# Performance work log

Measured on AMD Instinct MI355X. Metric: run time of the kernel, lower is better.

## Reference

```python
import jax, jax.numpy as jnp
import numpy as np
from jax import lax

B, T = 2, 2048
HID = 2048
H, K, KC = 16, 128, 4
D = H * K  # projection dim
EPS = 1e-5
SCALE = K ** -0.5


def causal_conv_silu(x, w, b):
    # x: [B,T,D], depthwise causal conv, w: [D,KC], b: [D]
    xp = jnp.pad(jnp.swapaxes(x, 1, 2), ((0, 0), (0, 0), (KC - 1, 0)))  # [B,D,T+KC-1]
    y = lax.conv_general_dilated(xp, w[:, None, :], (1,), 'VALID', feature_group_count=D)
    return jax.nn.silu(jnp.swapaxes(y, 1, 2) + b)


def l2norm(x):
    return x * lax.rsqrt(jnp.sum(x * x, -1, keepdims=True) + 1e-6)


def kda_scan(q, k, v, g, beta):
    # gated delta-rule linear recurrence (KDA), per-key-dim log decay g
    # q,k,v,g: [B,T,H,K]; beta: [B,T,H]
    qT, kT, vT, gT, bT = (jnp.moveaxis(a, 1, 0) for a in (q, k, v, g, beta))
    S0 = jnp.zeros((q.shape[0], H, K, K), q.dtype)  # state [B,H,K,V]

    def step(S, inp):
        qt, kt, vt, gt, bt = inp
        S = S * jnp.exp(gt)[..., None]                                   # decay along K
        vd = (vt - jnp.einsum('bhkv,bhk->bhv', S, kt)) * bt[..., None]   # delta-rule error * beta
        S = S + kt[..., None] * vd[:, :, None, :]                        # rank-1 update
        return S, jnp.einsum('bhkv,bhk->bhv', S, qt)

    _, o = lax.scan(step, S0, (qT, kT, vT, gT, bT))
    return jnp.moveaxis(o, 0, 1)  # [B,T,H,K]


def _forward(x, Wq, Wk, Wv, conv_q_w, conv_q_b, conv_k_w, conv_k_b, conv_v_w, conv_v_b,
             Wfa, Wfb, A_log, dt_bias, Wb, Wga, Wgb, o_norm_w, Wo):
    b, t = x.shape[:2]
    q = causal_conv_silu(x @ Wq, conv_q_w, conv_q_b).reshape(b, t, H, K)
    k = causal_conv_silu(x @ Wk, conv_k_w, conv_k_b).reshape(b, t, H, K)
    v = causal_conv_silu(x @ Wv, conv_v_w, conv_v_b).reshape(b, t, H, K)
    # fine-grained decay gate: g = -exp(A_log[h]) * softplus(f_b(f_a(x)) + dt_bias)
    g = jax.nn.softplus((x @ Wfa) @ Wfb + dt_bias).reshape(b, t, H, K)
    g = -jnp.exp(A_log)[None, None, :, None] * g
    beta = jax.nn.sigmoid(x @ Wb)  # [B,T,H]
    q = l2norm(q) * SCALE
    k = l2norm(k)
    o = kda_scan(q, k, v, g, beta)  # [B,T,H,K]
    # gated head-wise RMSNorm
    gate = ((x @ Wga) @ Wgb).reshape(b, t, H, K)
    var = jnp.mean(o * o, -1, keepdims=True)
    o = o * lax.rsqrt(var + EPS) * o_norm_w * jax.nn.sigmoid(gate)
    return o.reshape(b, t, D) @ Wo


def setup_inputs() -> dict:
    key = jax.random.key(0)
    ks = jax.random.split(key, 16)
    s = 0.02
    f32 = jnp.float32
    return {
        'x': jax.random.normal(ks[0], (B, T, HID), f32),
        'Wq': jax.random.normal(ks[1], (HID, D), f32) * s,
        'Wk': jax.random.normal(ks[2], (HID, D), f32) * s,
        'Wv': jax.random.normal(ks[3], (HID, D), f32) * s,
        'conv_q_w': jax.random.normal(ks[4], (D, KC), f32) * 0.2,
        'conv_q_b': jnp.zeros((D,), f32),
        'conv_k_w': jax.random.normal(ks[5], (D, KC), f32) * 0.2,
        'conv_k_b': jnp.zeros((D,), f32),
        'conv_v_w': jax.random.normal(ks[6], (D, KC), f32) * 0.2,
        'conv_v_b': jnp.zeros((D,), f32),
        'Wfa': jax.random.normal(ks[7], (HID, K), f32) * s,
        'Wfb': jax.random.normal(ks[8], (K, D), f32) * s,
        'A_log': jnp.log(jax.random.uniform(ks[9], (H,), f32, 1.0, 16.0)),
        'dt_bias': jnp.zeros((D,), f32),
        'Wb': jax.random.normal(ks[10], (HID, H), f32) * s,
        'Wga': jax.random.normal(ks[11], (HID, K), f32) * s,
        'Wgb': jax.random.normal(ks[12], (K, D), f32) * s,
        'o_norm_w': jnp.ones((K,), f32),
        'Wo': jax.random.normal(ks[13], (D, HID), f32) * s,
    }


def reference(x, Wq, Wk, Wv, conv_q_w, conv_q_b, conv_k_w, conv_k_b, conv_v_w, conv_v_b,
              Wfa, Wfb, A_log, dt_bias, Wb, Wga, Wgb, o_norm_w, Wo):
    return _forward(x, Wq, Wk, Wv, conv_q_w, conv_q_b, conv_k_w, conv_k_b, conv_v_w, conv_v_b,
                    Wfa, Wfb, A_log, dt_bias, Wb, Wga, Wgb, o_norm_w, Wo)
```

## Files before the change

### kernel.cpp

```cpp
#include <hip/hip_runtime.h>
#include <cstddef>

#define Bsz 2
#define Tt  2048
#define HIDc 2048
#define Hh  16
#define Kc  128
#define Dc  2048
#define BT  (Bsz*Tt)
#define TS  8
#define FGBs 384

typedef __attribute__((ext_vector_type(8))) __bf16 bf16x8;
typedef __attribute__((ext_vector_type(4))) __bf16 bf16x4;
typedef __attribute__((ext_vector_type(4))) float f32x4;

__device__ __forceinline__ float epilogue(float vacc, int c, int mode,
                                          const float* __restrict__ alog,
                                          const float* __restrict__ dtb) {
    if (mode == 1) {
        float z  = vacc + dtb[c];
        float sp = fmaxf(z, 0.f) + log1pf(expf(-fabsf(z)));
        return expf(-expf(alog[c >> 7]) * sp);
    } else if (mode == 3) {
        return (c >= 256) ? 1.f / (1.f + expf(-vacc)) : vacc;
    }
    return vacc;
}

__global__ __launch_bounds__(256) void gemm_bf16_mfma(
    const __bf16* __restrict__ A, const __bf16* __restrict__ Bw,
    float* __restrict__ C, __bf16* __restrict__ C2,
    int M, int N, int K, int lda, int mode,
    const float* __restrict__ alog, const float* __restrict__ dtb)
{
    __shared__ __bf16 As[128 * 64];
    __shared__ __bf16 Bs[128 * 64];
    const int tid = threadIdx.x;
    const int lane = tid & 63;
    const int wave = tid >> 6;
    const int wr = wave >> 1, wc = wave & 1;
    const int l15 = lane & 15, g = lane >> 4;
    const int row0 = blockIdx.y * 128, col0 = blockIdx.x * 128;

    f32x4 acc[4][4];
#pragma unroll
    for (int m = 0; m < 4; m++)
#pragma unroll
        for (int n = 0; n < 4; n++)
            acc[m][n] = (f32x4){0.f, 0.f, 0.f, 0.f};

    for (int k0 = 0; k0 < K; k0 += 64) {
        __syncthreads();
#pragma unroll
        for (int i = 0; i < 4; i++) {
            const int c = i * 256 + tid;
            const int row = c >> 3, kc = c & 7;
            const int scol = k0 + 8 * (kc ^ (row & 7));
            __builtin_amdgcn_global_load_lds(
                (const __attribute__((address_space(1))) void*)(A + (size_t)(row0 + row) * lda + scol),
                (__attribute__((address_space(3))) void*)(As + (size_t)(i * 256 + (tid & ~63)) * 8),
                16, 0, 0);
        }
#pragma unroll
        for (int i = 0; i < 4; i++) {
            const int c = i * 256 + tid;
            const int row = c >> 3, kc = c & 7;
            const int scol = k0 + 8 * (kc ^ (row & 7));
            __builtin_amdgcn_global_load_lds(
                (const __attribute__((address_space(1))) void*)(Bw + (size_t)(col0 + row) * K + scol),
                (__attribute__((address_space(3))) void*)(Bs + (size_t)(i * 256 + (tid & ~63)) * 8),
                16, 0, 0);
        }
        __syncthreads();
#pragma unroll
        for (int ks = 0; ks < 2; ks++) {
            bf16x8 af[4], bfr[4];
#pragma unroll
            for (int m = 0; m < 4; m++) {
                const int row = wr * 64 + m * 16 + l15;
                const int kc = ks * 4 + g;
                af[m] = *(const bf16x8*)(As + row * 64 + 8 * (kc ^ (row & 7)));
            }
#pragma unroll
            for (int n = 0; n < 4; n++) {
                const int col = wc * 64 + n * 16 + l15;
                const int kc = ks * 4 + g;
                bfr[n] = *(const bf16x8*)(Bs + col * 64 + 8 * (kc ^ (col & 7)));
            }
#pragma unroll
            for (int m = 0; m < 4; m++)
#pragma unroll
                for (int n = 0; n < 4; n++)
                    acc[m][n] = __builtin_amdgcn_mfma_f32_16x16x32_bf16(
                        af[m], bfr[n], acc[m][n], 0, 0, 0);
        }
    }
#pragma unroll
    for (int m = 0; m < 4; m++) {
        const int rbase = row0 + wr * 64 + m * 16 + g * 4;
#pragma unroll
        for (int n = 0; n < 4; n++) {
            const int col = col0 + wc * 64 + n * 16 + l15;
#pragma unroll
            for (int r = 0; r < 4; r++) {
                const float val = epilogue(acc[m][n][r], col, mode, alog, dtb);
                C[(size_t)(rbase + r) * N + col] = val;
                if (C2) C2[(size_t)(rbase + r) * N + col] = (__bf16)val;
            }
        }
    }
}

__global__ __launch_bounds__(256) void cvt_bf16(
    const float* __restrict__ in, __bf16* __restrict__ o)
{
    const int i = blockIdx.x * 256 + threadIdx.x;
    float4 v = *(const float4*)(in + (size_t)4 * i);
    bf16x4 r;
    r[0] = (__bf16)v.x; r[1] = (__bf16)v.y; r[2] = (__bf16)v.z; r[3] = (__bf16)v.w;
    *(bf16x4*)(o + (size_t)4 * i) = r;
}

__global__ __launch_bounds__(256) void transpose_to_bf16(
    const float* __restrict__ W, __bf16* __restrict__ WT, int Kd, int N)
{
    __shared__ float tile[32][33];
    const int n0 = blockIdx.x * 32, k0 = blockIdx.y * 32;
    const int tx = threadIdx.x & 31, ty = threadIdx.x >> 5;
#pragma unroll
    for (int i = 0; i < 4; i++)
        tile[ty + 8 * i][tx] = W[(size_t)(k0 + ty + 8 * i) * N + n0 + tx];
    __syncthreads();
#pragma unroll
    for (int i = 0; i < 4; i++)
        WT[(size_t)(n0 + ty + 8 * i) * Kd + k0 + tx] = (__bf16)tile[tx][ty + 8 * i];
}

__global__ __launch_bounds__(256) void pack_fgbT(
    const float* __restrict__ Wfa, const float* __restrict__ Wga,
    const float* __restrict__ Wb, __bf16* __restrict__ BcatT)
{
    const int i = blockIdx.x * 256 + threadIdx.x;
    if (i >= FGBs * HIDc) return;
    const int c = i / HIDc, k = i % HIDc;
    float v = 0.f;
    if (c < 128)      v = Wfa[(size_t)k * 128 + c];
    else if (c < 256) v = Wga[(size_t)k * 128 + (c - 128)];
    else if (c < 272) v = Wb[(size_t)k * 16 + (c - 256)];
    BcatT[i] = (__bf16)v;
}

__global__ __launch_bounds__(128) void conv_silu_norm(
    const float* __restrict__ pre, const float* __restrict__ cw,
    const float* __restrict__ cb, float* __restrict__ out, int mode)
{
    const int bid = blockIdx.x;
    const int h = bid & (Hh - 1);
    const int bt = bid >> 4;
    const int t = bt & (Tt - 1);
    const int lane = threadIdx.x;
    const int col = h * Kc + lane;
    const float w0 = cw[col * 4 + 0], w1 = cw[col * 4 + 1];
    const float w2 = cw[col * 4 + 2], w3 = cw[col * 4 + 3];
    const float* bp = pre + (size_t)bt * Dc + col;
    float acc = cb[col] + w3 * bp[0];
    if (t >= 1) acc += w2 * bp[-Dc];
    if (t >= 2) acc += w1 * bp[-2 * Dc];
    if (t >= 3) acc += w0 * bp[-3 * Dc];
    float val = acc / (1.f + expf(-acc));
    if (mode) {
        float ss = val * val;
#pragma unroll
        for (int m = 1; m < 64; m <<= 1) ss += __shfl_xor(ss, m);
        __shared__ float p2[2];
        if ((lane & 63) == 0) p2[lane >> 6] = ss;
        __syncthreads();
        float tot = p2[0] + p2[1];
        float r = rsqrtf(tot + 1e-6f);
        val *= r;
        if (mode == 2) val *= 0.08838834764831845f;
    }
    out[(size_t)bt * Dc + col] = val;
}

template <int CTRL>
__device__ __forceinline__ float dpp_add(float v) {
    return __int_as_float(__builtin_amdgcn_update_dpp(
        0, __float_as_int(v), CTRL, 0xf, 0xf, true));
}

__device__ __forceinline__ void reduce3_row(float& a, float& b, float& c) {
    a += dpp_add<0xB1>(a);
    b += dpp_add<0xB1>(b);
    c += dpp_add<0xB1>(c);
    a += dpp_add<0x4E>(a);
    b += dpp_add<0x4E>(b);
    c += dpp_add<0x4E>(c);
    a += dpp_add<0x124>(a);
    b += dpp_add<0x124>(b);
    c += dpp_add<0x124>(c);
    a += dpp_add<0x128>(a);
    b += dpp_add<0x128>(b);
    c += dpp_add<0x128>(c);
}

__device__ __forceinline__ float kda_step(
    const float4 cq[2], const float4 ck[2], const float4 cd[2],
    float cv, float cbt, float S[8])
{
    float kv0 = 0.f, kv1 = 0.f, qs0 = 0.f, qs1 = 0.f, qk0 = 0.f, qk1 = 0.f;
#pragma unroll
    for (int i = 0; i < 2; i++) {
        S[4 * i + 0] *= cd[i].x;
        S[4 * i + 1] *= cd[i].y;
        S[4 * i + 2] *= cd[i].z;
        S[4 * i + 3] *= cd[i].w;
        kv0 = fmaf(ck[i].x, S[4 * i + 0], kv0);
        kv1 = fmaf(ck[i].y, S[4 * i + 1], kv1);
        kv0 = fmaf(ck[i].z, S[4 * i + 2], kv0);
        kv1 = fmaf(ck[i].w, S[4 * i + 3], kv1);
        qs0 = fmaf(cq[i].x, S[4 * i + 0], qs0);
        qs1 = fmaf(cq[i].y, S[4 * i + 1], qs1);
        qs0 = fmaf(cq[i].z, S[4 * i + 2], qs0);
        qs1 = fmaf(cq[i].w, S[4 * i + 3], qs1);
        qk0 = fmaf(ck[i].x, cq[i].x, qk0);
        qk1 = fmaf(ck[i].y, cq[i].y, qk1);
        qk0 = fmaf(ck[i].z, cq[i].z, qk0);
        qk1 = fmaf(ck[i].w, cq[i].w, qk1);
    }
    float kv = kv0 + kv1, qs = qs0 + qs1, qk = qk0 + qk1;
    reduce3_row(kv, qs, qk);
    float vd = (cv - kv) * cbt;
    float ov = fmaf(qk, vd, qs);
#pragma unroll
    for (int i = 0; i < 2; i++) {
        S[4 * i + 0] = fmaf(ck[i].x, vd, S[4 * i + 0]);
        S[4 * i + 1] = fmaf(ck[i].y, vd, S[4 * i + 1]);
        S[4 * i + 2] = fmaf(ck[i].z, vd, S[4 * i + 2]);
        S[4 * i + 3] = fmaf(ck[i].w, vd, S[4 * i + 3]);
    }
    return ov;
}

__device__ __forceinline__ void kda_tile(
    const float (*sm)[TS * 128], const float* vm,
    const float* bm, float S[8], int kq, int vloc,
    float* __restrict__ op, int lane)
{
    float4 cq[2], ck[2], cd[2];
    float cv, cb;
#pragma unroll
    for (int i = 0; i < 2; i++) {
        cq[i] = *(const float4*)&sm[0][(kq * 2 + i) * 4];
        ck[i] = *(const float4*)&sm[1][(kq * 2 + i) * 4];
        cd[i] = *(const float4*)&sm[2][(kq * 2 + i) * 4];
    }
    cv = vm[vloc];
    cb = bm[0];
#pragma unroll
    for (int t = 0; t < TS; ++t) {
        float4 nq[2], nk[2], nd[2];
        float nv = 0.f, nb = 0.f;
        if (t + 1 < TS) {
#pragma unroll
            for (int i = 0; i < 2; i++) {
                nq[i] = *(const float4*)&sm[0][(t + 1) * 128 + (kq * 2 + i) * 4];
                nk[i] = *(const float4*)&sm[1][(t + 1) * 128 + (kq * 2 + i) * 4];
                nd[i] = *(const float4*)&sm[2][(t + 1) * 128 + (kq * 2 + i) * 4];
            }
            nv = vm[(t + 1) * 4 + vloc];
            nb = bm[t + 1];
        }
        const float ov = kda_step(cq, ck, cd, cv, cb, S);
        if ((lane & 15) == 0)
            op[(size_t)t * Dc + vloc] = ov;
        if (t + 1 < TS) {
#pragma unroll
            for (int i = 0; i < 2; i++) { cq[i] = nq[i]; ck[i] = nk[i]; cd[i] = nd[i]; }
            cv = nv; cb = nb;
        }
    }
}

__global__ __launch_bounds__(64, 2) void kda_scan_kernel(
    const float* __restrict__ q, const float* __restrict__ k,
    const float* __restrict__ v, const float* __restrict__ dec,
    const float* __restrict__ fgb, float* __restrict__ o)
{
    __shared__ float sA[3][TS * 128];
    __shared__ float sB[3][TS * 128];
    __shared__ float sC[3][TS * 128];
    __shared__ float vA[TS * 4], vB[TS * 4], vC[TS * 4];
    __shared__ float bA[TS], bB[TS], bC[TS];

    const int bid = blockIdx.x;
    const int r8 = bid & 7;
    const int s = bid >> 3;
    const int bh = r8 + 8 * (s >> 5);
    const int vc = s & 31;
    const int h = bh & (Hh - 1);
    const int b = bh >> 4;
    const int lane = threadIdx.x;
    const int vloc = lane >> 4;
    const int kq = lane & 15;
    const size_t base = ((size_t)b * Tt) * Dc + h * Kc;
    const size_t bbase = ((size_t)b * Tt) * FGBs + 256 + h;

    float S[8];
#pragma unroll
    for (int i = 0; i < 8; i++) S[i] = 0.f;

    const int s_t = lane >> 5;
    const int s_w = lane & 31;

#define STAGE(TILE, SM, VM, BM)                                                 \
    {                                                                           \
        _Pragma("unroll")                                                       \
        for (int r = 0; r < 4; r++) {                                           \
            const size_t rb = base + (size_t)((TILE) * TS + 2 * r + s_t) * Dc   \
                              + s_w * 4;                                        \
            __builtin_amdgcn_global_load_lds(                                   \
                (const __attribute__((address_space(1))) void*)(q + rb),        \
                (__attribute__((address_space(3))) void*)(&SM[0][r * 256]),     \
                16, 0, 0);                                                      \
            __builtin_amdgcn_global_load_lds(                                   \
                (const __attribute__((address_space(1))) void*)(k + rb),        \
                (__attribute__((address_space(3))) void*)(&SM[1][r * 256]),     \
                16, 0, 0);                                                      \
            __builtin_amdgcn_global_load_lds(                                   \
                (const __attribute__((address_space(1))) void*)(dec + rb),      \
                (__attribute__((address_space(3))) void*)(&SM[2][r * 256]),     \
                16, 0, 0);                                                      \
        }                                                                       \
        if (lane < 32)                                                          \
            __builtin_amdgcn_global_load_lds(                                   \
                (const __attribute__((address_space(1))) void*)(v + base        \
                    + (size_t)((TILE) * TS + (lane >> 2)) * Dc + vc * 4         \
                    + (lane & 3)),                                              \
                (__attribute__((address_space(3))) void*)(&VM[0]), 4, 0, 0);    \
        if (lane < TS)                                                          \
            __builtin_amdgcn_global_load_lds(                                   \
                (const __attribute__((address_space(1))) void*)(fgb + bbase     \
                    + (size_t)((TILE) * TS + lane) * FGBs),                     \
                (__attribute__((address_space(3))) void*)(&BM[0]), 4, 0, 0);    \
    }

    STAGE(0, sA, vA, bA);
    STAGE(1, sB, vB, bB);
    asm volatile("s_waitcnt vmcnt(14)" ::: "memory");
    __builtin_amdgcn_sched_barrier(0);

    const int NT = Tt / TS;
    for (int tile = 0; tile < NT; ++tile) {
        if (tile + 2 < NT) {
            const int r2 = (tile + 2) % 3;
            float (*sT)[TS * 128] = (r2 == 0) ? sA : (r2 == 1) ? sB : sC;
            float* vT = (r2 == 0) ? vA : (r2 == 1) ? vB : vC;
            float* bT = (r2 == 0) ? bA : (r2 == 1) ? bB : bC;
            STAGE(tile + 2, sT, vT, bT);
            __builtin_amdgcn_sched_barrier(0);
        }
        const int rr = tile % 3;
        const float (*sm)[TS * 128] = (rr == 0) ? sA : (rr == 1) ? sB : sC;
        const float* vm = (rr == 0) ? vA : (rr == 1) ? vB : vC;
        const float* bm = (rr == 0) ? bA : (rr == 1) ? bB : bC;
        kda_tile(sm, vm, bm, S, kq, vloc,
                 o + base + (size_t)tile * TS * Dc + vc * 4, lane);
        if (tile + 2 < NT)
            asm volatile("s_waitcnt vmcnt(22)" ::: "memory");
        else
            asm volatile("s_waitcnt vmcnt(8)" ::: "memory");
        __builtin_amdgcn_sched_barrier(0);
    }
#undef STAGE
}

__global__ __launch_bounds__(128) void post_norm(
    const float* __restrict__ o, const float* __restrict__ gate,
    const float* __restrict__ onw, __bf16* __restrict__ og)
{
    const int bid = blockIdx.x;
    const int h = bid & (Hh - 1);
    const int bt = bid >> 4;
    const int lane = threadIdx.x;
    size_t idx = (size_t)bt * Dc + h * Kc + lane;
    float ov = o[idx];
    float ss = ov * ov;
#pragma unroll
    for (int m = 1; m < 64; m <<= 1) ss += __shfl_xor(ss, m);
    __shared__ float p2[2];
    if ((lane & 63) == 0) p2[lane >> 6] = ss;
    __syncthreads();
    float var = (p2[0] + p2[1]) * (1.f / 128.f);
    float r = rsqrtf(var + 1e-5f);
    float gt = gate[idx];
    og[idx] = (__bf16)(ov * r * onw[lane] * (1.f / (1.f + expf(-gt))));
}

extern "C" void kernel_launch(void* const* d_in, const int* in_sizes, int n_in,
                              void* d_out, int out_size, void* d_ws, size_t ws_size,
                              hipStream_t stream) {
    const float* x        = (const float*)d_in[0];
    const float* Wq       = (const float*)d_in[1];
    const float* Wk       = (const float*)d_in[2];
    const float* Wv       = (const float*)d_in[3];
    const float* conv_q_w = (const float*)d_in[4];
    const float* conv_q_b = (const float*)d_in[5];
    const float* conv_k_w = (const float*)d_in[6];
    const float* conv_k_b = (const float*)d_in[7];
    const float* conv_v_w = (const float*)d_in[8];
    const float* conv_v_b = (const float*)d_in[9];
    const float* Wfa      = (const float*)d_in[10];
    const float* Wfb      = (const float*)d_in[11];
    const float* A_log    = (const float*)d_in[12];
    const float* dt_bias  = (const float*)d_in[13];
    const float* Wb       = (const float*)d_in[14];
    const float* Wga      = (const float*)d_in[15];
    const float* Wgb      = (const float*)d_in[16];
    const float* o_norm_w = (const float*)d_in[17];
    const float* Wo       = (const float*)d_in[18];
    float* out = (float*)d_out;

    float* ws = (float*)d_ws;
    const size_t SZ = (size_t)BT * Dc;
    float* bufA = ws + 0 * SZ;
    float* bufB = ws + 1 * SZ;
    float* bufC = ws + 2 * SZ;
    float* bufG = ws + 3 * SZ;
    float* bufQ = ws + 4 * SZ;
    float* bufI = ws + 5 * SZ;
    float* fgb  = ws + 6 * SZ;
    __bf16* fgb16 = (__bf16*)(fgb + (size_t)BT * FGBs);
    __bf16* xb    = fgb16 + (size_t)BT * FGBs;
    __bf16* wT    = xb + SZ;
    __bf16* BcatT = wT + (size_t)HIDc * Dc;

    dim3 blk(256);
    cvt_bf16<<<dim3(SZ / 1024), blk, 0, stream>>>(x, xb);
    pack_fgbT<<<dim3((FGBs * HIDc + 255) / 256), blk, 0, stream>>>(Wfa, Wga, Wb, BcatT);
    dim3 tgrid(Dc / 32, HIDc / 32);
    dim3 gbig(Dc / 128, BT / 128);
    transpose_to_bf16<<<tgrid, blk, 0, stream>>>(Wq, wT, HIDc, Dc);
    gemm_bf16_mfma<<<gbig, blk, 0, stream>>>(xb, wT, bufA, nullptr, BT, Dc, HIDc, HIDc, 0, nullptr, nullptr);
    transpose_to_bf16<<<tgrid, blk, 0, stream>>>(Wk, wT, HIDc, Dc);
    gemm_bf16_mfma<<<gbig, blk, 0, stream>>>(xb, wT, bufB, nullptr, BT, Dc, HIDc, HIDc, 0, nullptr, nullptr);
    transpose_to_bf16<<<tgrid, blk, 0, stream>>>(Wv, wT, HIDc, Dc);
    gemm_bf16_mfma<<<gbig, blk, 0, stream>>>(xb, wT, bufC, nullptr, BT, Dc, HIDc, HIDc, 0, nullptr, nullptr);
    dim3 gskin(FGBs / 128, BT / 128);
    gemm_bf16_mfma<<<gskin, blk, 0, stream>>>(xb, BcatT, fgb, fgb16, BT, FGBs, HIDc, HIDc, 3, nullptr, nullptr);
    dim3 tskin(Dc / 32, Kc / 32);
    transpose_to_bf16<<<tskin, blk, 0, stream>>>(Wfb, wT, Kc, Dc);
    gemm_bf16_mfma<<<gbig, blk, 0, stream>>>(fgb16, wT, bufG, nullptr, BT, Dc, Kc, FGBs, 1, A_log, dt_bias);
    transpose_to_bf16<<<tskin, blk, 0, stream>>>(Wgb, wT, Kc, Dc);
    gemm_bf16_mfma<<<gbig, blk, 0, stream>>>(fgb16 + 128, wT, bufI, nullptr, BT, Dc, Kc, FGBs, 0, nullptr, nullptr);
    dim3 cblk(128);
    dim3 cgrid(BT * Hh);
    conv_silu_norm<<<cgrid, cblk, 0, stream>>>(bufA, conv_q_w, conv_q_b, bufQ, 2);
    conv_silu_norm<<<cgrid, cblk, 0, stream>>>(bufB, conv_k_w, conv_k_b, bufA, 1);
    conv_silu_norm<<<cgrid, cblk, 0, stream>>>(bufC, conv_v_w, conv_v_b, bufB, 0);
    kda_scan_kernel<<<dim3(1024), dim3(64), 0, stream>>>(bufQ, bufA, bufB, bufG, fgb, bufC);
    post_norm<<<cgrid, cblk, 0, stream>>>(bufC, bufI, o_norm_w, xb);
    transpose_to_bf16<<<tgrid, blk, 0, stream>>>(Wo, wT, Dc, HIDc);
    dim3 gout(HIDc / 128, BT / 128);
    gemm_bf16_mfma<<<gout, blk, 0, stream>>>(xb, wT, out, nullptr, BT, HIDc, Dc, Dc, 0, nullptr, nullptr);
}
```

Baseline: 944.0 us.

## Batch QKV transposes and GEMMs into single launches; swizzle scan LDS reads

Merges the three Wq/Wk/Wv weight transposes and the three projection GEMMs into one launch each, using blockIdx.z to select the weight and output buffer. This gives a single 3x-larger grid that fills the GPU better and removes launch gaps. Separately, the scan kernel rotates each lane's LDS float4 slot by vloc to reduce bank conflicts among the four v-groups reading the same row. The cost is three transposed weight copies held in the workspace at once instead of one reused buffer.

Result: no change. 928.5 us (-1.6%).

```diff
diff --git a/kernel.cpp b/kernel.cpp
--- a/kernel.cpp
+++ b/kernel.cpp
@@ -29,13 +29,15 @@
 }
 
 __global__ __launch_bounds__(256) void gemm_bf16_mfma(
-    const __bf16* __restrict__ A, const __bf16* __restrict__ Bw,
-    float* __restrict__ C, __bf16* __restrict__ C2,
+    const __bf16* __restrict__ A, const __bf16* __restrict__ BwB, size_t bz,
+    float* __restrict__ CB, size_t cz, __bf16* __restrict__ C2,
     int M, int N, int K, int lda, int mode,
     const float* __restrict__ alog, const float* __restrict__ dtb)
 {
     __shared__ __bf16 As[128 * 64];
     __shared__ __bf16 Bs[128 * 64];
+    const __bf16* Bw = BwB + (size_t)blockIdx.z * bz;
+    float* C = CB + (size_t)blockIdx.z * cz;
     const int tid = threadIdx.x;
     const int lane = tid & 63;
     const int wave = tid >> 6;
@@ -126,6 +128,25 @@
     const float* __restrict__ W, __bf16* __restrict__ WT, int Kd, int N)
 {
     __shared__ float tile[32][33];
+    const int n0 = blockIdx.x * 32, k0 = blockIdx.y * 32;
+    const int tx = threadIdx.x & 31, ty = threadIdx.x >> 5;
+#pragma unroll
+    for (int i = 0; i < 4; i++)
+        tile[ty + 8 * i][tx] = W[(size_t)(k0 + ty + 8 * i) * N + n0 + tx];
+    __syncthreads();
+#pragma unroll
+    for (int i = 0; i < 4; i++)
+        WT[(size_t)(n0 + ty + 8 * i) * Kd + k0 + tx] = (__bf16)tile[tx][ty + 8 * i];
+}
+
+__global__ __launch_bounds__(256) void transpose3_to_bf16(
+    const float* __restrict__ W0, const float* __restrict__ W1,
+    const float* __restrict__ W2, __bf16* __restrict__ WTB, size_t wz,
+    int Kd, int N)
+{
+    __shared__ float tile[32][33];
+    const float* W = (blockIdx.z == 0) ? W0 : (blockIdx.z == 1) ? W1 : W2;
+    __bf16* WT = WTB + (size_t)blockIdx.z * wz;
     const int n0 = blockIdx.x * 32, k0 = blockIdx.y * 32;
     const int tx = threadIdx.x & 31, ty = threadIdx.x >> 5;
 #pragma unroll
@@ -245,17 +266,17 @@
 
 __device__ __forceinline__ void kda_tile(
     const float (*sm)[TS * 128], const float* vm,
-    const float* bm, float S[8], int kq, int vloc,
+    const float* bm, float S[8], int sl0, int sl1, int vloc,
     float* __restrict__ op, int lane)
 {
     float4 cq[2], ck[2], cd[2];
     float cv, cb;
-#pragma unroll
-    for (int i = 0; i < 2; i++) {
-        cq[i] = *(const float4*)&sm[0][(kq * 2 + i) * 4];
-        ck[i] = *(const float4*)&sm[1][(kq * 2 + i) * 4];
-        cd[i] = *(const float4*)&sm[2][(kq * 2 + i) * 4];
-    }
+    cq[0] = *(const float4*)&sm[0][sl0];
+    ck[0] = *(const float4*)&sm[1][sl0];
+    cd[0] = *(const float4*)&sm[2][sl0];
+    cq[1] = *(const float4*)&sm[0][sl1];
+    ck[1] = *(const float4*)&sm[1][sl1];
+    cd[1] = *(const float4*)&sm[2][sl1];
     cv = vm[vloc];
     cb = bm[0];
 #pragma unroll
@@ -263,12 +284,12 @@
         float4 nq[2], nk[2], nd[2];
         float nv = 0.f, nb = 0.f;
         if (t + 1 < TS) {
-#pragma unroll
-            for (int i = 0; i < 2; i++) {
-                nq[i] = *(const float4*)&sm[0][(t + 1) * 128 + (kq * 2 + i) * 4];
-                nk[i] = *(const float4*)&sm[1][(t + 1) * 128 + (kq * 2 + i) * 4];
-                nd[i] = *(const float4*)&sm[2][(t + 1) * 128 + (kq * 2 + i) * 4];
-            }
+            nq[0] = *(const float4*)&sm[0][(t + 1) * 128 + sl0];
+            nk[0] = *(const float4*)&sm[1][(t + 1) * 128 + sl0];
+            nd[0] = *(const float4*)&sm[2][(t + 1) * 128 + sl0];
+            nq[1] = *(const float4*)&sm[0][(t + 1) * 128 + sl1];
+            nk[1] = *(const float4*)&sm[1][(t + 1) * 128 + sl1];
+            nd[1] = *(const float4*)&sm[2][(t + 1) * 128 + sl1];
             nv = vm[(t + 1) * 4 + vloc];
             nb = bm[t + 1];
         }
@@ -304,6 +325,8 @@
     const int lane = threadIdx.x;
     const int vloc = lane >> 4;
     const int kq = lane & 15;
+    const int sl0 = ((kq * 2 + 0 + vloc) & 31) * 4;
+    const int sl1 = ((kq * 2 + 1 + vloc) & 31) * 4;
     const size_t base = ((size_t)b * Tt) * Dc + h * Kc;
     const size_t bbase = ((size_t)b * Tt) * FGBs + 256 + h;
 
@@ -365,7 +388,7 @@
         const float (*sm)[TS * 128] = (rr == 0) ? sA : (rr == 1) ? sB : sC;
         const float* vm = (rr == 0) ? vA : (rr == 1) ? vB : vC;
         const float* bm = (rr == 0) ? bA : (rr == 1) ? bB : bC;
-        kda_tile(sm, vm, bm, S, kq, vloc,
+        kda_tile(sm, vm, bm, S, sl0, sl1, vloc,
                  o + base + (size_t)tile * TS * Dc + vc * 4, lane);
         if (tile + 2 < NT)
             asm volatile("s_waitcnt vmcnt(22)" ::: "memory");
@@ -433,27 +456,29 @@
     float* fgb  = ws + 6 * SZ;
     __bf16* fgb16 = (__bf16*)(fgb + (size_t)BT * FGBs);
     __bf16* xb    = fgb16 + (size_t)BT * FGBs;
-    __bf16* wT    = xb + SZ;
-    __bf16* BcatT = wT + (size_t)HIDc * Dc;
+    __bf16* wT3   = xb + SZ;
+    __bf16* BcatT = wT3 + (size_t)3 * HIDc * Dc;
+    const size_t WZ = (size_t)HIDc * Dc;
 
     dim3 blk(256);
     cvt_bf16<<<dim3(SZ / 1024), blk, 0, stream>>>(x, xb);
     pack_fgbT<<<dim3((FGBs * HIDc + 255) / 256), blk, 0, stream>>>(Wfa, Wga, Wb, BcatT);
-    dim3 tgrid(Dc / 32, HIDc / 32);
-    dim3 gbig(Dc / 128, BT / 128);
-    transpose_to_bf16<<<tgrid, blk, 0, stream>>>(Wq, wT, HIDc, Dc);
-    gemm_bf16_mfma<<<gbig, blk, 0, stream>>>(xb, wT, bufA, nullptr, BT, Dc, HIDc, HIDc, 0, nullptr, nullptr);
-    transpose_to_bf16<<<tgrid, blk, 0, stream>>>(Wk, wT, HIDc, Dc);
-    gemm_bf16_mfma<<<gbig, blk, 0, stream>>>(xb, wT, bufB, nullptr, BT, Dc, HIDc, HIDc, 0, nullptr, nullptr);
-    transpose_to_bf16<<<tgrid, blk, 0, stream>>>(Wv, wT, HIDc, Dc);
-    gemm_bf16_mfma<<<gbig, blk, 0, stream>>>(xb, wT, bufC, nullptr, BT, Dc, HIDc, HIDc, 0, nullptr, nullptr);
-    dim3 gskin(FGBs / 128, BT / 128);
-    gemm_bf16_mfma<<<gskin, blk, 0, stream>>>(xb, BcatT, fgb, fgb16, BT, FGBs, HIDc, HIDc, 3, nullptr, nullptr);
+    dim3 tgrid3(Dc / 32, HIDc / 32, 3);
+    transpose3_to_bf16<<<tgrid3, blk, 0, stream>>>(Wq, Wk, Wv, wT3, WZ, HIDc, Dc);
+    dim3 gbig3(Dc / 128, BT / 128, 3);
+    gemm_bf16_mfma<<<gbig3, blk, 0, stream>>>(xb, wT3, WZ, bufA, SZ, nullptr,
+                                              BT, Dc, HIDc, HIDc, 0, nullptr, nullptr);
+    dim3 gskin(FGBs / 128, BT / 128, 1);
+    gemm_bf16_mfma<<<gskin, blk, 0, stream>>>(xb, BcatT, 0, fgb, 0, fgb16,
+                                              BT, FGBs, HIDc, HIDc, 3, nullptr, nullptr);
     dim3 tskin(Dc / 32, Kc / 32);
-    transpose_to_bf16<<<tskin, blk, 0, stream>>>(Wfb, wT, Kc, Dc);
-    gemm_bf16_mfma<<<gbig, blk, 0, stream>>>(fgb16, wT, bufG, nullptr, BT, Dc, Kc, FGBs, 1, A_log, dt_bias);
-    transpose_to_bf16<<<tskin, blk, 0, stream>>>(Wgb, wT, Kc, Dc);
-    gemm_bf16_mfma<<<gbig, blk, 0, stream>>>(fgb16 + 128, wT, bufI, nullptr, BT, Dc, Kc, FGBs, 0, nullptr, nullptr);
+    dim3 gbig(Dc / 128, BT / 128, 1);
+    transpose_to_bf16<<<tskin, blk, 0, stream>>>(Wfb, wT3, Kc, Dc);
+    gemm_bf16_mfma<<<gbig, blk, 0, stream>>>(fgb16, wT3, 0, bufG, 0, nullptr,
+                                             BT, Dc, Kc, FGBs, 1, A_log, dt_bias);
+    transpose_to_bf16<<<tskin, blk, 0, stream>>>(Wgb, wT3, Kc, Dc);
+    gemm_bf16_mfma<<<gbig, blk, 0, stream>>>(fgb16 + 128, wT3, 0, bufI, 0, nullptr,
+                                             BT, Dc, Kc, FGBs, 0, nullptr, nullptr);
     dim3 cblk(128);
     dim3 cgrid(BT * Hh);
     conv_silu_norm<<<cgrid, cblk, 0, stream>>>(bufA, conv_q_w, conv_q_b, bufQ, 2);
@@ -461,7 +486,9 @@
     conv_silu_norm<<<cgrid, cblk, 0, stream>>>(bufC, conv_v_w, conv_v_b, bufB, 0);
     kda_scan_kernel<<<dim3(1024), dim3(64), 0, stream>>>(bufQ, bufA, bufB, bufG, fgb, bufC);
     post_norm<<<cgrid, cblk, 0, stream>>>(bufC, bufI, o_norm_w, xb);
-    transpose_to_bf16<<<tgrid, blk, 0, stream>>>(Wo, wT, Dc, HIDc);
-    dim3 gout(HIDc / 128, BT / 128);
-    gemm_bf16_mfma<<<gout, blk, 0, stream>>>(xb, wT, out, nullptr, BT, HIDc, Dc, Dc, 0, nullptr, nullptr);
-}
+    dim3 tgrid(Dc / 32, HIDc / 32);
+    transpose_to_bf16<<<tgrid, blk, 0, stream>>>(Wo, wT3, Dc, HIDc);
+    dim3 gout(HIDc / 128, BT / 128, 1);
+    gemm_bf16_mfma<<<gout, blk, 0, stream>>>(xb, wT3, 0, out, 0, nullptr,
+                                             BT, HIDc, Dc, Dc, 0, nullptr, nullptr);
+}
```
